# Kernel optimization log

Measured on AMD Instinct MI355X. Metric: run time of the kernel, lower is better.

## Reference

```python
import jax, jax.numpy as jnp
import numpy as np

B, E, N1, K, CIN, CB, COUT, G = 2, 2048, 96, 32, 64, 32, 64, 4
NEG_SLOPE = 0.01  # nn.LeakyReLU default


def setup_inputs() -> dict:
    key = jax.random.key(0)
    ks = jax.random.split(key, 9)
    sites1 = jax.random.normal(ks[0], (B, N1, CIN), jnp.float32)
    sites2 = jax.random.normal(ks[1], (B, K, CIN), jnp.float32)
    bonds = jax.random.normal(ks[2], (B, E, CB), jnp.float32)
    idx1 = jax.random.randint(ks[3], (E,), 0, N1, jnp.int32)
    idx2 = jax.random.randint(ks[4], (E,), 0, K, jnp.int32)
    idx2_oh = jax.nn.one_hot(idx2, K, dtype=jnp.float32)  # [E, K]
    F = 2 * CIN + CB
    W_eq = jax.random.normal(ks[5], (G, F, COUT), jnp.float32) / np.float32(np.sqrt(F))
    b_eq = jnp.zeros((COUT,), jnp.float32)
    W_att = jax.random.normal(ks[6], (COUT, 1), jnp.float32) / np.float32(np.sqrt(COUT))
    b_att = jnp.zeros((1,), jnp.float32)
    # permutation group action on the K cells: identity + random perms
    perms = [jnp.arange(K, dtype=jnp.int32)]
    pk = ks[7]
    for _ in range(G - 1):
        pk, sk = jax.random.split(pk)
        perms.append(jax.random.permutation(sk, K).astype(jnp.int32))
    perms1 = jnp.stack(perms)  # [G, K]
    perms2 = perms1            # same action on input and output cell axes
    return dict(sites1=sites1, sites2=sites2, bonds=bonds, W_eq=W_eq, b_eq=b_eq,
                W_att=W_att, b_att=b_att, idx2_oh=idx2_oh, idx1=idx1, idx2=idx2,
                perms1=perms1, perms2=perms2)


def reference(sites1, sites2, bonds, W_eq, b_eq, W_att, b_att, idx2_oh, idx1, idx2, perms1, perms2):
    Bn = sites1.shape[0]
    Gn, Kn = perms1.shape
    On = W_eq.shape[2]
    # gather sender / receiver site features along the site axis
    sites_s = jnp.take(sites1, idx1, axis=1)              # [B,E,CIN]
    sites_r = jnp.take(sites2, idx2, axis=1)              # [B,E,CIN]
    vectors = jnp.concatenate([sites_s, sites_r, bonds], axis=2)  # [B,E,F]
    # outer-product expansion onto cells (idx2_oh is one-hot over K)
    vc = jnp.einsum('bef,ek->befk', vectors, idx2_oh)     # [B,E,F,K]
    # permutation-equivariant linear (group-averaged): per-group-element weight,
    # input cells permuted by perms1, output cells un-permuted by perms2
    xg = vc[:, :, :, perms1]                               # [B,E,F,G,K]
    yg = jnp.einsum('befgk,gfo->beogk', xg, W_eq)          # [B,E,O,G,K]
    inv2 = jnp.argsort(perms2, axis=1)                     # inverse perms [G,K]
    garr = jnp.arange(Gn)[:, None]
    y = yg[:, :, :, garr, inv2].mean(axis=3)               # [B,E,O,K]
    y = jax.nn.leaky_relu(y + b_eq[None, None, :, None], NEG_SLOPE)
    # gather each edge's receiving cell slot == dot with one-hot
    lat = jnp.einsum('beok,ek->beo', y, idx2_oh)           # [B,E,O]
    att = jax.nn.sigmoid(jnp.einsum('beo,oj->bej', lat, W_att) + b_att)  # [B,E,1]
    lat = att * lat
    # scatter_add over edges into receiving sites
    out = jnp.zeros((Bn, Kn, On), lat.dtype).at[:, idx2].add(lat)  # [B,K,O]
    return out
```

## Files before the change

### kernel.cpp

```cpp
#include <hip/hip_runtime.h>
#include <math.h>

#define Bn   2
#define En   2048
#define N1n  96
#define Kn   32
#define CINn 64
#define CBn  32
#define On   64
#define Gn   4
#define Fn   160
#define NEG  0.01f

__global__ void weff_kernel(const float* __restrict__ W_eq,
                            const int* __restrict__ perms1,
                            const int* __restrict__ perms2,
                            float* __restrict__ Weff) {
    const int FO = Fn * On;
    int idx = blockIdx.x * blockDim.x + threadIdx.x;
    if (idx >= Kn * FO) return;
    int k = idx / FO;
    int r = idx - k * FO;
    float s = 0.f;
#pragma unroll
    for (int g = 0; g < Gn; ++g) {
        int j = 0;
        for (; j < Kn; ++j) if (perms2[g * Kn + j] == k) break;
        float wg = (j < Kn && perms1[g * Kn + j] == k) ? 1.f : 0.f;
        s += wg * W_eq[g * FO + r];
    }
    Weff[idx] = 0.25f * s;
}

template <bool USE_WEFF>
__global__ void __launch_bounds__(64)
edge_kernel(const float* __restrict__ sites1, const float* __restrict__ sites2,
            const float* __restrict__ bonds,  const float* __restrict__ W,
            const float* __restrict__ b_eq,   const float* __restrict__ W_att,
            const float* __restrict__ b_att,  const int* __restrict__ idx1,
            const int* __restrict__ idx2,     const int* __restrict__ perms1,
            const int* __restrict__ perms2,   float* __restrict__ out) {
    const int t  = threadIdx.x;
    const int be = blockIdx.x;
    const int b  = be >> 11;
    const int e  = be & (En - 1);

    __shared__ float v[Fn];
    __shared__ float wgs[Gn];

    const int i1 = idx1[e];
    const int k2 = idx2[e];

    v[t]        = sites1[(b * N1n + i1) * CINn + t];
    v[CINn + t] = sites2[(b * Kn  + k2) * CINn + t];
    if (t < CBn) v[2 * CINn + t] = bonds[(b * En + e) * CBn + t];

    if (!USE_WEFF && t < Gn) {
        int g = t, j = 0;
        for (; j < Kn; ++j) if (perms2[g * Kn + j] == k2) break;
        wgs[g] = (j < Kn && perms1[g * Kn + j] == k2) ? 1.f : 0.f;
    }
    __syncthreads();

    const int og = t & 15;
    const int fg = t >> 4;

    float4 acc = make_float4(0.f, 0.f, 0.f, 0.f);
    if (USE_WEFF) {
        const float4* Wk = (const float4*)(W + (size_t)k2 * Fn * On);
#pragma unroll 4
        for (int f = fg; f < Fn; f += 4) {
            float  vf = v[f];
            float4 w  = Wk[f * 16 + og];
            acc.x += vf * w.x; acc.y += vf * w.y;
            acc.z += vf * w.z; acc.w += vf * w.w;
        }
    } else {
        const float w0 = wgs[0], w1 = wgs[1], w2 = wgs[2], w3 = wgs[3];
        const float4* W4 = (const float4*)W;
#pragma unroll 2
        for (int f = fg; f < Fn; f += 4) {
            float  vf = 0.25f * v[f];
            float4 a0 = W4[(0 * Fn + f) * 16 + og];
            float4 a1 = W4[(1 * Fn + f) * 16 + og];
            float4 a2 = W4[(2 * Fn + f) * 16 + og];
            float4 a3 = W4[(3 * Fn + f) * 16 + og];
            acc.x += vf * (w0 * a0.x + w1 * a1.x + w2 * a2.x + w3 * a3.x);
            acc.y += vf * (w0 * a0.y + w1 * a1.y + w2 * a2.y + w3 * a3.y);
            acc.z += vf * (w0 * a0.z + w1 * a1.z + w2 * a2.z + w3 * a3.z);
            acc.w += vf * (w0 * a0.w + w1 * a1.w + w2 * a2.w + w3 * a3.w);
        }
    }

#pragma unroll
    for (int m = 16; m <= 32; m <<= 1) {
        acc.x += __shfl_xor(acc.x, m);
        acc.y += __shfl_xor(acc.y, m);
        acc.z += __shfl_xor(acc.z, m);
        acc.w += __shfl_xor(acc.w, m);
    }

    const float4 be4 = ((const float4*)b_eq)[og];
    float4 lat;
    lat.x = acc.x + be4.x; lat.x = lat.x > 0.f ? lat.x : NEG * lat.x;
    lat.y = acc.y + be4.y; lat.y = lat.y > 0.f ? lat.y : NEG * lat.y;
    lat.z = acc.z + be4.z; lat.z = lat.z > 0.f ? lat.z : NEG * lat.z;
    lat.w = acc.w + be4.w; lat.w = lat.w > 0.f ? lat.w : NEG * lat.w;

    const float4 wa = ((const float4*)W_att)[og];
    float part = lat.x * wa.x + lat.y * wa.y + lat.z * wa.z + lat.w * wa.w;
#pragma unroll
    for (int m = 1; m <= 8; m <<= 1) part += __shfl_xor(part, m);

    const float att = 1.f / (1.f + expf(-(part + b_att[0])));

    if (fg == 0) {
        float* op = out + ((size_t)b * Kn + k2) * On + og * 4;
        atomicAdd(op + 0, att * lat.x);
        atomicAdd(op + 1, att * lat.y);
        atomicAdd(op + 2, att * lat.z);
        atomicAdd(op + 3, att * lat.w);
    }
}

extern "C" void kernel_launch(void* const* d_in, const int* in_sizes, int n_in,
                              void* d_out, int out_size, void* d_ws, size_t ws_size,
                              hipStream_t stream) {
    const float* sites1 = (const float*)d_in[0];
    const float* sites2 = (const float*)d_in[1];
    const float* bonds  = (const float*)d_in[2];
    const float* W_eq   = (const float*)d_in[3];
    const float* b_eq   = (const float*)d_in[4];
    const float* W_att  = (const float*)d_in[5];
    const float* b_att  = (const float*)d_in[6];
    const int*   idx1   = (const int*)d_in[8];
    const int*   idx2   = (const int*)d_in[9];
    const int*   perms1 = (const int*)d_in[10];
    const int*   perms2 = (const int*)d_in[11];
    float* out = (float*)d_out;

    hipMemsetAsync(out, 0, (size_t)out_size * sizeof(float), stream);

    const size_t weff_bytes = (size_t)Kn * Fn * On * sizeof(float);
    if (ws_size >= weff_bytes) {
        float* Weff = (float*)d_ws;
        const int total = Kn * Fn * On;
        weff_kernel<<<(total + 255) / 256, 256, 0, stream>>>(W_eq, perms1, perms2, Weff);
        edge_kernel<true><<<Bn * En, 64, 0, stream>>>(
            sites1, sites2, bonds, Weff, b_eq, W_att, b_att,
            idx1, idx2, perms1, perms2, out);
    } else {
        edge_kernel<false><<<Bn * En, 64, 0, stream>>>(
            sites1, sites2, bonds, W_eq, b_eq, W_att, b_att,
            idx1, idx2, perms1, perms2, out);
    }
}
```

Baseline: 103.5 us.

## Fuse into one kernel per (batch, cell) with shared-memory Weff and no atomics

Replaces the weff precompute kernel, memset and per-edge kernel with a single kernel that launches one block per (batch, receiving cell). Each block builds its cell's effective weight in LDS, scans idx2 to collect the edges that target that cell, and processes them with eight waves. Per-wave results are reduced in shared memory and written directly, which removes the global atomics and the extra launches. The cost is a grid of only 64 blocks, a serial 2048-entry scan in every block, and load imbalance when cells receive different numbers of edges.

```diff
diff --git a/kernel.cpp b/kernel.cpp
--- a/kernel.cpp
+++ b/kernel.cpp
@@ -11,115 +11,124 @@
 #define Gn   4
 #define Fn   160
 #define NEG  0.01f
+#define NW   8
+#define NT   (NW * 64)
 
-__global__ void weff_kernel(const float* __restrict__ W_eq,
-                            const int* __restrict__ perms1,
-                            const int* __restrict__ perms2,
-                            float* __restrict__ Weff) {
-    const int FO = Fn * On;
-    int idx = blockIdx.x * blockDim.x + threadIdx.x;
-    if (idx >= Kn * FO) return;
-    int k = idx / FO;
-    int r = idx - k * FO;
-    float s = 0.f;
-#pragma unroll
-    for (int g = 0; g < Gn; ++g) {
-        int j = 0;
-        for (; j < Kn; ++j) if (perms2[g * Kn + j] == k) break;
-        float wg = (j < Kn && perms1[g * Kn + j] == k) ? 1.f : 0.f;
-        s += wg * W_eq[g * FO + r];
-    }
-    Weff[idx] = 0.25f * s;
-}
+__global__ void __launch_bounds__(NT, 1)
+fused_kernel(const float* __restrict__ sites1, const float* __restrict__ sites2,
+             const float* __restrict__ bonds,  const float* __restrict__ W_eq,
+             const float* __restrict__ b_eq,   const float* __restrict__ W_att,
+             const float* __restrict__ b_att,  const int* __restrict__ idx1,
+             const int* __restrict__ idx2,     const int* __restrict__ perms1,
+             const int* __restrict__ perms2,   float* __restrict__ out) {
+    __shared__ float Weff[Fn][On];
+    __shared__ float vbuf[NW][Fn];
+    __shared__ float red[NW][On];
+    __shared__ float s2[CINn];
+    __shared__ float wgs[Gn];
+    __shared__ int   elist[En];
+    __shared__ int   ecount;
 
-template <bool USE_WEFF>
-__global__ void __launch_bounds__(64)
-edge_kernel(const float* __restrict__ sites1, const float* __restrict__ sites2,
-            const float* __restrict__ bonds,  const float* __restrict__ W,
-            const float* __restrict__ b_eq,   const float* __restrict__ W_att,
-            const float* __restrict__ b_att,  const int* __restrict__ idx1,
-            const int* __restrict__ idx2,     const int* __restrict__ perms1,
-            const int* __restrict__ perms2,   float* __restrict__ out) {
     const int t  = threadIdx.x;
-    const int be = blockIdx.x;
-    const int b  = be >> 11;
-    const int e  = be & (En - 1);
+    const int bk = blockIdx.x;
+    const int b  = bk >> 5;
+    const int k2 = bk & (Kn - 1);
 
-    __shared__ float v[Fn];
-    __shared__ float wgs[Gn];
-
-    const int i1 = idx1[e];
-    const int k2 = idx2[e];
-
-    v[t]        = sites1[(b * N1n + i1) * CINn + t];
-    v[CINn + t] = sites2[(b * Kn  + k2) * CINn + t];
-    if (t < CBn) v[2 * CINn + t] = bonds[(b * En + e) * CBn + t];
-
-    if (!USE_WEFF && t < Gn) {
+    if (t < Gn) {
         int g = t, j = 0;
         for (; j < Kn; ++j) if (perms2[g * Kn + j] == k2) break;
         wgs[g] = (j < Kn && perms1[g * Kn + j] == k2) ? 1.f : 0.f;
     }
+    if (t == Gn) ecount = 0;
     __syncthreads();
 
-    const int og = t & 15;
-    const int fg = t >> 4;
-
-    float4 acc = make_float4(0.f, 0.f, 0.f, 0.f);
-    if (USE_WEFF) {
-        const float4* Wk = (const float4*)(W + (size_t)k2 * Fn * On);
-#pragma unroll 4
-        for (int f = fg; f < Fn; f += 4) {
-            float  vf = v[f];
-            float4 w  = Wk[f * 16 + og];
-            acc.x += vf * w.x; acc.y += vf * w.y;
-            acc.z += vf * w.z; acc.w += vf * w.w;
-        }
-    } else {
+    {
         const float w0 = wgs[0], w1 = wgs[1], w2 = wgs[2], w3 = wgs[3];
-        const float4* W4 = (const float4*)W;
-#pragma unroll 2
-        for (int f = fg; f < Fn; f += 4) {
-            float  vf = 0.25f * v[f];
-            float4 a0 = W4[(0 * Fn + f) * 16 + og];
-            float4 a1 = W4[(1 * Fn + f) * 16 + og];
-            float4 a2 = W4[(2 * Fn + f) * 16 + og];
-            float4 a3 = W4[(3 * Fn + f) * 16 + og];
-            acc.x += vf * (w0 * a0.x + w1 * a1.x + w2 * a2.x + w3 * a3.x);
-            acc.y += vf * (w0 * a0.y + w1 * a1.y + w2 * a2.y + w3 * a3.y);
-            acc.z += vf * (w0 * a0.z + w1 * a1.z + w2 * a2.z + w3 * a3.z);
-            acc.w += vf * (w0 * a0.w + w1 * a1.w + w2 * a2.w + w3 * a3.w);
+        const float4* W4 = (const float4*)W_eq;
+        float4* Wd = (float4*)&Weff[0][0];
+        const int n4 = Fn * On / 4;
+        for (int i = t; i < n4; i += NT) {
+            float4 a0 = W4[i], a1 = W4[n4 + i], a2 = W4[2 * n4 + i], a3 = W4[3 * n4 + i];
+            float4 r;
+            r.x = 0.25f * (w0 * a0.x + w1 * a1.x + w2 * a2.x + w3 * a3.x);
+            r.y = 0.25f * (w0 * a0.y + w1 * a1.y + w2 * a2.y + w3 * a3.y);
+            r.z = 0.25f * (w0 * a0.z + w1 * a1.z + w2 * a2.z + w3 * a3.z);
+            r.w = 0.25f * (w0 * a0.w + w1 * a1.w + w2 * a2.w + w3 * a3.w);
+            Wd[i] = r;
         }
     }
 
+    for (int e = t; e < En; e += NT)
+        if (idx2[e] == k2) { int p = atomicAdd(&ecount, 1); elist[p] = e; }
+
+    if (t < CINn) s2[t] = sites2[(b * Kn + k2) * CINn + t];
+    __syncthreads();
+
+    const int w    = t >> 6;
+    const int lane = t & 63;
+    const int og   = lane & 15;
+    const int fg   = lane >> 4;
+
+    const float4 be4 = ((const float4*)b_eq)[og];
+    const float4 wa  = ((const float4*)W_att)[og];
+    const float  ba  = b_att[0];
+    const int    ec  = ecount;
+
+    float4 oacc = make_float4(0.f, 0.f, 0.f, 0.f);
+
+    for (int i = w; i < ec; i += NW) {
+        const int e  = elist[i];
+        const int i1 = idx1[e];
+
+        vbuf[w][lane]        = sites1[(b * N1n + i1) * CINn + lane];
+        vbuf[w][CINn + lane] = s2[lane];
+        if (lane < CBn) vbuf[w][2 * CINn + lane] = bonds[(b * En + e) * CBn + lane];
+        __builtin_amdgcn_wave_barrier();
+
+        float4 acc = make_float4(0.f, 0.f, 0.f, 0.f);
 #pragma unroll
-    for (int m = 16; m <= 32; m <<= 1) {
-        acc.x += __shfl_xor(acc.x, m);
-        acc.y += __shfl_xor(acc.y, m);
-        acc.z += __shfl_xor(acc.z, m);
-        acc.w += __shfl_xor(acc.w, m);
+        for (int fi = 0; fi < Fn / 4; ++fi) {
+            const int f = 4 * fi + fg;
+            const float  vf = vbuf[w][f];
+            const float4 wv = *(const float4*)&Weff[f][og * 4];
+            acc.x += vf * wv.x; acc.y += vf * wv.y;
+            acc.z += vf * wv.z; acc.w += vf * wv.w;
+        }
+        __builtin_amdgcn_wave_barrier();
+
+#pragma unroll
+        for (int m = 16; m <= 32; m <<= 1) {
+            acc.x += __shfl_xor(acc.x, m);
+            acc.y += __shfl_xor(acc.y, m);
+            acc.z += __shfl_xor(acc.z, m);
+            acc.w += __shfl_xor(acc.w, m);
+        }
+
+        float4 lat;
+        lat.x = acc.x + be4.x; lat.x = lat.x > 0.f ? lat.x : NEG * lat.x;
+        lat.y = acc.y + be4.y; lat.y = lat.y > 0.f ? lat.y : NEG * lat.y;
+        lat.z = acc.z + be4.z; lat.z = lat.z > 0.f ? lat.z : NEG * lat.z;
+        lat.w = acc.w + be4.w; lat.w = lat.w > 0.f ? lat.w : NEG * lat.w;
+
+        float part = lat.x * wa.x + lat.y * wa.y + lat.z * wa.z + lat.w * wa.w;
+#pragma unroll
+        for (int m = 1; m <= 8; m <<= 1) part += __shfl_xor(part, m);
+
+        const float att = 1.f / (1.f + expf(-(part + ba)));
+        oacc.x += att * lat.x;
+        oacc.y += att * lat.y;
+        oacc.z += att * lat.z;
+        oacc.w += att * lat.w;
     }
 
-    const float4 be4 = ((const float4*)b_eq)[og];
-    float4 lat;
-    lat.x = acc.x + be4.x; lat.x = lat.x > 0.f ? lat.x : NEG * lat.x;
-    lat.y = acc.y + be4.y; lat.y = lat.y > 0.f ? lat.y : NEG * lat.y;
-    lat.z = acc.z + be4.z; lat.z = lat.z > 0.f ? lat.z : NEG * lat.z;
-    lat.w = acc.w + be4.w; lat.w = lat.w > 0.f ? lat.w : NEG * lat.w;
+    if (fg == 0) *(float4*)&red[w][og * 4] = oacc;
+    __syncthreads();
 
-    const float4 wa = ((const float4*)W_att)[og];
-    float part = lat.x * wa.x + lat.y * wa.y + lat.z * wa.z + lat.w * wa.w;
+    if (t < On) {
+        float s = 0.f;
 #pragma unroll
-    for (int m = 1; m <= 8; m <<= 1) part += __shfl_xor(part, m);
-
-    const float att = 1.f / (1.f + expf(-(part + b_att[0])));
-
-    if (fg == 0) {
-        float* op = out + ((size_t)b * Kn + k2) * On + og * 4;
-        atomicAdd(op + 0, att * lat.x);
-        atomicAdd(op + 1, att * lat.y);
-        atomicAdd(op + 2, att * lat.z);
-        atomicAdd(op + 3, att * lat.w);
+        for (int q = 0; q < NW; ++q) s += red[q][t];
+        out[((size_t)b * Kn + k2) * On + t] = s;
     }
 }
 
@@ -139,19 +148,7 @@
     const int*   perms2 = (const int*)d_in[11];
     float* out = (float*)d_out;
 
-    hipMemsetAsync(out, 0, (size_t)out_size * sizeof(float), stream);
-
-    const size_t weff_bytes = (size_t)Kn * Fn * On * sizeof(float);
-    if (ws_size >= weff_bytes) {
-        float* Weff = (float*)d_ws;
-        const int total = Kn * Fn * On;
-        weff_kernel<<<(total + 255) / 256, 256, 0, stream>>>(W_eq, perms1, perms2, Weff);
-        edge_kernel<true><<<Bn * En, 64, 0, stream>>>(
-            sites1, sites2, bonds, Weff, b_eq, W_att, b_att,
-            idx1, idx2, perms1, perms2, out);
-    } else {
-        edge_kernel<false><<<Bn * En, 64, 0, stream>>>(
-            sites1, sites2, bonds, W_eq, b_eq, W_att, b_att,
-            idx1, idx2, perms1, perms2, out);
-    }
+    fused_kernel<<<Bn * Kn, NT, 0, stream>>>(
+        sites1, sites2, bonds, W_eq, b_eq, W_att, b_att,
+        idx1, idx2, perms1, perms2, out);
 }
```

New measurement: 100.0 us. 1.04x faster.
